# Performance work log

Hardware: AMD Instinct MI355X
Metric: run time of the kernel (lower is better)

The kernel has to match this reference:

```python
import jax, jax.numpy as jnp
import numpy as np

B, T = 2, 2048
D_MODEL, D_HIDDEN = 1024, 2048
N_EXPERTS, TOP_K = 8, 2
N_TOKENS = B * T
CAPACITY = 2 * N_TOKENS * TOP_K // N_EXPERTS  # 4096


def setup_inputs() -> dict:
    key = jax.random.key(0)
    k_x, k_rw, k_w, k_v, k_o = jax.random.split(key, 5)
    x = jax.random.normal(k_x, (B, T, D_MODEL), jnp.float32)
    # router: nn.Linear(d_model, n_experts) -> weight [E, D], bias [E]
    router_w = jax.random.normal(k_rw, (N_EXPERTS, D_MODEL), jnp.float32) * D_MODEL ** -0.5
    router_b = jnp.zeros((N_EXPERTS,), jnp.float32)
    # stacked expert params, matching SwiGLU init scales
    W = jax.random.normal(k_w, (N_EXPERTS, D_MODEL, D_HIDDEN), jnp.float32) * D_MODEL ** -0.5
    V = jax.random.normal(k_v, (N_EXPERTS, D_MODEL, D_HIDDEN), jnp.float32) * D_MODEL ** -0.5
    W_out = jax.random.normal(k_o, (N_EXPERTS, D_HIDDEN, D_MODEL), jnp.float32) * D_HIDDEN ** -0.5
    return {"x": x, "router_w": router_w, "router_b": router_b, "W": W, "V": V, "W_out": W_out}


def reference(x, router_w, router_b, W, V, W_out):
    Bq, Tq, D = x.shape
    N = Bq * Tq
    x_flat = x.reshape(N, D)

    # token-level top-k routing
    router_logits = x_flat @ router_w.T + router_b            # [N, E]
    top_vals, top_ids = jax.lax.top_k(router_logits, TOP_K)   # [N, K]
    top_probs = jax.nn.softmax(top_vals, axis=-1)             # [N, K]

    # pad row N: gathers with fill index N read zeros / contribute zero weight
    x_pad = jnp.concatenate([x_flat, jnp.zeros((1, D), x_flat.dtype)], axis=0)
    probs_pad = jnp.concatenate([top_probs, jnp.zeros((1, TOP_K), top_probs.dtype)], axis=0)

    out = jnp.zeros((N + 1, D), x_flat.dtype)
    for e in range(N_EXPERTS):  # static small loop over experts
        tok, slot = jnp.nonzero(top_ids == e, size=CAPACITY, fill_value=(N, 0))
        w = probs_pad[tok, slot][:, None]     # [C, 1], zero for padding slots
        xin = x_pad[tok]                      # [C, D] gather
        a = xin @ W[e]                        # [C, H]
        b = xin @ V[e]                        # [C, H]
        y = (a * (b * jax.nn.sigmoid(b))) @ W_out[e]  # SwiGLU: a * swish(b) -> [C, D]
        out = out.at[tok].add(y * w)          # weighted scatter-add
    return out[:N].reshape(Bq, Tq, D)
```

## Files before the change

### kernel.cpp

```cpp
#include <hip/hip_runtime.h>
#include <cstdint>
#include <cstddef>

#define N_TOK 4096
#define DM    1024
#define DH    2048
#define NE    8
#define NSLOT 8192

typedef short bf16x8_t __attribute__((ext_vector_type(8)));
typedef float f32x4    __attribute__((ext_vector_type(4)));
typedef unsigned short u16x8 __attribute__((ext_vector_type(8)));

__device__ __forceinline__ unsigned short f2bf(float f) {
  union { float f; unsigned int u; } v; v.f = f;
  unsigned int u = v.u;
  u += 0x7fffu + ((u >> 16) & 1u);
  return (unsigned short)(u >> 16);
}

#define GLD16(gp, lp)                                                          \
  __builtin_amdgcn_global_load_lds(                                            \
      (const __attribute__((address_space(1))) void*)(gp),                     \
      (__attribute__((address_space(3))) void*)(lp), 16, 0, 0)

__global__ __launch_bounds__(256) void k_transpose_bf16(
    const float* __restrict__ src0, const float* __restrict__ src1,
    unsigned short* __restrict__ dst, int R, int C,
    long srcEStride, long dstEStride, int rowOff1) {
  const int z = blockIdx.z;
  const int e = z & 7;
  const bool second = z >= 8;
  const float* s = (second ? src1 : src0) + (size_t)e * srcEStride;
  unsigned short* d = dst + (size_t)e * dstEStride + (size_t)(second ? rowOff1 : 0) * R;
  const int c0 = blockIdx.x * 64, r0 = blockIdx.y * 64;
  __shared__ float tile[64][65];
  const int t = threadIdx.x;
  {
    const int cc = (t & 15) * 4;
#pragma unroll
    for (int j = 0; j < 4; j++) {
      const int r = (t >> 4) + j * 16;
      const float4 v = *(const float4*)(s + (size_t)(r0 + r) * C + c0 + cc);
      tile[r][cc + 0] = v.x; tile[r][cc + 1] = v.y;
      tile[r][cc + 2] = v.z; tile[r][cc + 3] = v.w;
    }
  }
  __syncthreads();
  {
    const int r8 = (t & 7) * 8;
#pragma unroll
    for (int j = 0; j < 2; j++) {
      const int c = (t >> 3) + j * 32;
      u16x8 o;
#pragma unroll
      for (int i = 0; i < 8; i++) o[i] = f2bf(tile[r8 + i][c]);
      *(u16x8*)(d + (size_t)(c0 + c) * R + r0 + r8) = o;
    }
  }
}

__global__ __launch_bounds__(256) void k_router(
    const float* __restrict__ x, const float* __restrict__ rw,
    const float* __restrict__ rb, int* __restrict__ counts,
    int* __restrict__ meta_e, int* __restrict__ meta_idx,
    float* __restrict__ meta_p) {
  const int wv = threadIdx.x >> 6;
  const int l  = threadIdx.x & 63;
  const int tk = blockIdx.x * 4 + wv;
  const float* xr = x + (size_t)tk * DM;

  float acc[NE];
#pragma unroll
  for (int e = 0; e < NE; e++) acc[e] = 0.f;
#pragma unroll 4
  for (int i = 0; i < DM / 64; i++) {
    const float xv = xr[i * 64 + l];
#pragma unroll
    for (int e = 0; e < NE; e++) acc[e] += xv * rw[e * DM + i * 64 + l];
  }
#pragma unroll
  for (int off = 32; off > 0; off >>= 1) {
#pragma unroll
    for (int e = 0; e < NE; e++) acc[e] += __shfl_xor(acc[e], off);
  }
#pragma unroll
  for (int e = 0; e < NE; e++) acc[e] += rb[e];

  float v0 = -1e30f; int e0 = 0;
#pragma unroll
  for (int e = 0; e < NE; e++) { if (acc[e] > v0) { v0 = acc[e]; e0 = e; } }
  float v1 = -1e30f; int e1 = 0;
#pragma unroll
  for (int e = 0; e < NE; e++) { if (e != e0 && acc[e] > v1) { v1 = acc[e]; e1 = e; } }
  const float p0 = 1.0f / (1.0f + __expf(v1 - v0));
  const float p1 = 1.0f - p0;

  if (l == 0) {
    const int i0 = atomicAdd(&counts[e0], 1);
    const int i1 = atomicAdd(&counts[e1], 1);
    meta_e[tk * 2 + 0] = e0;  meta_e[tk * 2 + 1] = e1;
    meta_idx[tk * 2 + 0] = i0; meta_idx[tk * 2 + 1] = i1;
    meta_p[tk * 2 + 0] = p0;  meta_p[tk * 2 + 1] = p1;
  }
}

__global__ void k_prefix(const int* __restrict__ counts, int* __restrict__ offsets) {
  if (threadIdx.x == 0) {
    int s = 0;
#pragma unroll
    for (int e = 0; e < NE; e++) { offsets[e] = s; s += counts[e]; }
  }
}

__global__ __launch_bounds__(256) void k_gather(
    const float* __restrict__ x, const int* __restrict__ meta_e,
    const int* __restrict__ meta_idx, const int* __restrict__ offsets,
    unsigned short* __restrict__ Xg) {
  const int s = blockIdx.x;
  const int tk = s >> 1;
  const int e = meta_e[s];
  const int gslot = offsets[e] + meta_idx[s];
  const float4 v = ((const float4*)(x + (size_t)tk * DM))[threadIdx.x];
  ushort4 o;
  o.x = f2bf(v.x); o.y = f2bf(v.y); o.z = f2bf(v.z); o.w = f2bf(v.w);
  *(ushort4*)(Xg + (size_t)gslot * DM + threadIdx.x * 4) = o;
}

__global__ __launch_bounds__(256, 2) void k_gemm1(
    const unsigned short* __restrict__ Xg, const unsigned short* __restrict__ B1t,
    unsigned short* __restrict__ G, const int* __restrict__ counts,
    const int* __restrict__ offsets) {
  const int e = blockIdx.z;
  const int mt = blockIdx.y;
  const int cnt = counts[e];
  if (mt * 128 >= cnt) return;
  const int h0 = blockIdx.x * 128;
  const int off = offsets[e];
  const int row_base = off + mt * 128;

  __shared__ unsigned short As[128 * 32];
  __shared__ unsigned short Ws[128 * 32];
  __shared__ unsigned short Vs[128 * 32];

  const int t = threadIdx.x;
  const int l = t & 63;
  const int w = t >> 6;
  const int wm = (w >> 1) * 64;
  const int wn = (w & 1) * 64;
  const int lr = l & 15;
  const int kq = (l >> 4) * 8;

  const unsigned short* Bw = B1t + ((size_t)e * 4096 + h0) * DM;
  const unsigned short* Bv = Bw + (size_t)DH * DM;

  const int c0 = t, c1 = t + 256;
  const int ar0 = c0 >> 2, ak0 = (c0 & 3) * 8;
  const int ar1 = c1 >> 2, ak1 = (c1 & 3) * 8;
  const int arow0 = min(row_base + ar0, NSLOT - 1);
  const int arow1 = min(row_base + ar1, NSLOT - 1);

  f32x4 acc_a[4][4], acc_b[4][4];
  const f32x4 z4 = {0.f, 0.f, 0.f, 0.f};
#pragma unroll
  for (int i = 0; i < 4; i++)
#pragma unroll
    for (int j = 0; j < 4; j++) { acc_a[i][j] = z4; acc_b[i][j] = z4; }

  for (int k0 = 0; k0 < DM; k0 += 32) {
    __syncthreads();
    GLD16(Xg + (size_t)arow0 * DM + k0 + ak0, As + c0 * 8);
    GLD16(Xg + (size_t)arow1 * DM + k0 + ak1, As + c1 * 8);
    GLD16(Bw + (size_t)ar0 * DM + k0 + ak0, Ws + c0 * 8);
    GLD16(Bw + (size_t)ar1 * DM + k0 + ak1, Ws + c1 * 8);
    GLD16(Bv + (size_t)ar0 * DM + k0 + ak0, Vs + c0 * 8);
    GLD16(Bv + (size_t)ar1 * DM + k0 + ak1, Vs + c1 * 8);
    __syncthreads();

    bf16x8_t af[4], wf[4], vf[4];
#pragma unroll
    for (int mi = 0; mi < 4; mi++)
      af[mi] = *(const bf16x8_t*)&As[(wm + mi * 16 + lr) * 32 + kq];
#pragma unroll
    for (int ni = 0; ni < 4; ni++) {
      wf[ni] = *(const bf16x8_t*)&Ws[(wn + ni * 16 + lr) * 32 + kq];
      vf[ni] = *(const bf16x8_t*)&Vs[(wn + ni * 16 + lr) * 32 + kq];
    }
#pragma unroll
    for (int mi = 0; mi < 4; mi++)
#pragma unroll
      for (int ni = 0; ni < 4; ni++) {
        acc_a[mi][ni] = __builtin_amdgcn_mfma_f32_16x16x32_bf16(af[mi], wf[ni], acc_a[mi][ni], 0, 0, 0);
        acc_b[mi][ni] = __builtin_amdgcn_mfma_f32_16x16x32_bf16(af[mi], vf[ni], acc_b[mi][ni], 0, 0, 0);
      }
  }

  const int q4 = (l >> 4) * 4;
#pragma unroll
  for (int mi = 0; mi < 4; mi++) {
#pragma unroll
    for (int r = 0; r < 4; r++) {
      const int mloc = mt * 128 + wm + mi * 16 + q4 + r;
      if (mloc >= cnt) continue;
      unsigned short* grow = G + (size_t)(off + mloc) * DH;
#pragma unroll
      for (int ni = 0; ni < 4; ni++) {
        const int h = h0 + wn + ni * 16 + lr;
        const float a = acc_a[mi][ni][r];
        const float b = acc_b[mi][ni][r];
        const float s = b / (1.0f + __expf(-b));
        grow[h] = f2bf(a * s);
      }
    }
  }
}

__global__ __launch_bounds__(256, 2) void k_gemm2(
    const unsigned short* __restrict__ G, const unsigned short* __restrict__ B2t,
    float* __restrict__ Y, const int* __restrict__ counts,
    const int* __restrict__ offsets) {
  const int e = blockIdx.z;
  const int mt = blockIdx.y;
  const int cnt = counts[e];
  if (mt * 128 >= cnt) return;
  const int n0 = blockIdx.x * 128;
  const int off = offsets[e];
  const int row_base = off + mt * 128;

  __shared__ unsigned short As[128 * 32];
  __shared__ unsigned short Bs[128 * 32];

  const int t = threadIdx.x;
  const int l = t & 63;
  const int w = t >> 6;
  const int wm = (w >> 1) * 64;
  const int wn = (w & 1) * 64;
  const int lr = l & 15;
  const int kq = (l >> 4) * 8;

  const unsigned short* Bp = B2t + ((size_t)e * DM + n0) * DH;

  const int c0 = t, c1 = t + 256;
  const int ar0 = c0 >> 2, ak0 = (c0 & 3) * 8;
  const int ar1 = c1 >> 2, ak1 = (c1 & 3) * 8;
  const int arow0 = min(row_base + ar0, NSLOT - 1);
  const int arow1 = min(row_base + ar1, NSLOT - 1);

  f32x4 acc[4][4];
  const f32x4 z4 = {0.f, 0.f, 0.f, 0.f};
#pragma unroll
  for (int i = 0; i < 4; i++)
#pragma unroll
    for (int j = 0; j < 4; j++) acc[i][j] = z4;

  for (int k0 = 0; k0 < DH; k0 += 32) {
    __syncthreads();
    GLD16(G + (size_t)arow0 * DH + k0 + ak0, As + c0 * 8);
    GLD16(G + (size_t)arow1 * DH + k0 + ak1, As + c1 * 8);
    GLD16(Bp + (size_t)ar0 * DH + k0 + ak0, Bs + c0 * 8);
    GLD16(Bp + (size_t)ar1 * DH + k0 + ak1, Bs + c1 * 8);
    __syncthreads();

    bf16x8_t af[4], bf[4];
#pragma unroll
    for (int mi = 0; mi < 4; mi++)
      af[mi] = *(const bf16x8_t*)&As[(wm + mi * 16 + lr) * 32 + kq];
#pragma unroll
    for (int ni = 0; ni < 4; ni++)
      bf[ni] = *(const bf16x8_t*)&Bs[(wn + ni * 16 + lr) * 32 + kq];
#pragma unroll
    for (int mi = 0; mi < 4; mi++)
#pragma unroll
      for (int ni = 0; ni < 4; ni++)
        acc[mi][ni] = __builtin_amdgcn_mfma_f32_16x16x32_bf16(af[mi], bf[ni], acc[mi][ni], 0, 0, 0);
  }

  const int q4 = (l >> 4) * 4;
#pragma unroll
  for (int mi = 0; mi < 4; mi++) {
#pragma unroll
    for (int r = 0; r < 4; r++) {
      const int mloc = mt * 128 + wm + mi * 16 + q4 + r;
      if (mloc >= cnt) continue;
      float* yrow = Y + (size_t)(off + mloc) * DM;
#pragma unroll
      for (int ni = 0; ni < 4; ni++)
        yrow[n0 + wn + ni * 16 + lr] = acc[mi][ni][r];
    }
  }
}

__global__ __launch_bounds__(256) void k_combine(
    const float* __restrict__ Y, const int* __restrict__ meta_e,
    const int* __restrict__ meta_idx, const float* __restrict__ meta_p,
    const int* __restrict__ offsets, float* __restrict__ out) {
  const int tk = blockIdx.x;
  const int s0 = tk * 2, s1 = s0 + 1;
  const int g0 = offsets[meta_e[s0]] + meta_idx[s0];
  const int g1 = offsets[meta_e[s1]] + meta_idx[s1];
  const float w0 = meta_p[s0], w1 = meta_p[s1];
  const float4 a = ((const float4*)(Y + (size_t)g0 * DM))[threadIdx.x];
  const float4 b = ((const float4*)(Y + (size_t)g1 * DM))[threadIdx.x];
  float4 o;
  o.x = w0 * a.x + w1 * b.x;
  o.y = w0 * a.y + w1 * b.y;
  o.z = w0 * a.z + w1 * b.z;
  o.w = w0 * a.w + w1 * b.w;
  ((float4*)(out + (size_t)tk * DM))[threadIdx.x] = o;
}

extern "C" void kernel_launch(void* const* d_in, const int* in_sizes, int n_in,
                              void* d_out, int out_size, void* d_ws, size_t ws_size,
                              hipStream_t stream) {
  const float* x    = (const float*)d_in[0];
  const float* rw   = (const float*)d_in[1];
  const float* rb   = (const float*)d_in[2];
  const float* W    = (const float*)d_in[3];
  const float* V    = (const float*)d_in[4];
  const float* Wout = (const float*)d_in[5];
  float* out = (float*)d_out;

  char* p = (char*)d_ws;
  unsigned short* B1t = (unsigned short*)p; p += (size_t)NE * 4096 * DM * 2;
  float*          Y   = (float*)B1t;
  unsigned short* B2t = (unsigned short*)p; p += (size_t)NE * DM * DH * 2;
  unsigned short* Xg  = (unsigned short*)p; p += (size_t)NSLOT * DM * 2;
  unsigned short* G   = (unsigned short*)p; p += (size_t)NSLOT * DH * 2;
  int*   counts      = (int*)p;   p += 256;
  int*   offsets     = (int*)p;   p += 256;
  int*   meta_e      = (int*)p;   p += (size_t)N_TOK * 2 * 4;
  int*   meta_idx    = (int*)p;   p += (size_t)N_TOK * 2 * 4;
  float* meta_p      = (float*)p; p += (size_t)N_TOK * 2 * 4;

  hipMemsetAsync(counts, 0, 256, stream);

  k_transpose_bf16<<<dim3(DH / 64, DM / 64, 2 * NE), 256, 0, stream>>>(
      W, V, B1t, DM, DH, (long)DM * DH, (long)4096 * DM, DH);
  k_transpose_bf16<<<dim3(DM / 64, DH / 64, NE), 256, 0, stream>>>(
      Wout, Wout, B2t, DH, DM, (long)DH * DM, (long)DM * DH, 0);

  k_router<<<N_TOK / 4, 256, 0, stream>>>(x, rw, rb, counts, meta_e, meta_idx, meta_p);
  k_prefix<<<1, 64, 0, stream>>>(counts, offsets);
  k_gather<<<NSLOT, 256, 0, stream>>>(x, meta_e, meta_idx, offsets, Xg);

  k_gemm1<<<dim3(DH / 128, NSLOT / 128, NE), 256, 0, stream>>>(Xg, B1t, G, counts, offsets);
  k_gemm2<<<dim3(DM / 128, NSLOT / 128, NE), 256, 0, stream>>>(G, B2t, Y, counts, offsets);
  k_combine<<<N_TOK, 256, 0, stream>>>(Y, meta_e, meta_idx, meta_p, offsets, out);
}
```

Measured before the change: 532.9 us.

## Split-K the down-projection GEMM and fold launches into fewer kernels

Splits gemm2's K dimension into two halves written to separate Y buffers, doubling the block count for better CU occupancy, with the combine kernel summing both halves. Merges the two weight transposes into one launch that also zeroes the counts, removes the memset and the prefix kernel by computing offsets inline from counts, and gathers once per token to both slots. The split costs an extra fp32 Y buffer of write and read traffic in exchange for more parallelism and fewer launches.

```diff
diff --git a/kernel.cpp b/kernel.cpp
--- a/kernel.cpp
+++ b/kernel.cpp
@@ -24,16 +24,39 @@
       (const __attribute__((address_space(1))) void*)(gp),                     \
       (__attribute__((address_space(3))) void*)(lp), 16, 0, 0)
 
-__global__ __launch_bounds__(256) void k_transpose_bf16(
-    const float* __restrict__ src0, const float* __restrict__ src1,
-    unsigned short* __restrict__ dst, int R, int C,
-    long srcEStride, long dstEStride, int rowOff1) {
+__device__ __forceinline__ int expert_off(const int* __restrict__ counts, int e, int* cnt) {
+  int off = 0, s = 0;
+#pragma unroll
+  for (int i = 0; i < NE; i++) { if (i == e) off = s; s += counts[i]; }
+  *cnt = counts[e];
+  return off;
+}
+
+__global__ __launch_bounds__(256) void k_transpose(
+    const float* __restrict__ W, const float* __restrict__ V,
+    const float* __restrict__ Wout, unsigned short* __restrict__ B1t,
+    unsigned short* __restrict__ B2t, int* __restrict__ counts) {
+  if (blockIdx.z == 0 && blockIdx.x == 0 && blockIdx.y == 0 && threadIdx.x < NE)
+    counts[threadIdx.x] = 0;
+
   const int z = blockIdx.z;
-  const int e = z & 7;
-  const bool second = z >= 8;
-  const float* s = (second ? src1 : src0) + (size_t)e * srcEStride;
-  unsigned short* d = dst + (size_t)e * dstEStride + (size_t)(second ? rowOff1 : 0) * R;
-  const int c0 = blockIdx.x * 64, r0 = blockIdx.y * 64;
+  const float* s;
+  unsigned short* d;
+  int R, C, xt, yt;
+  if (z < 16) {
+    const int e = z & 7;
+    s = ((z < 8) ? W : V) + (size_t)e * DM * DH;
+    d = B1t + (size_t)e * 4096 * DM + (size_t)((z < 8) ? 0 : DH) * DM;
+    R = DM; C = DH; xt = blockIdx.x; yt = blockIdx.y;
+  } else {
+    const int e = z - 16;
+    s = Wout + (size_t)e * DH * DM;
+    d = B2t + (size_t)e * DM * DH;
+    R = DH; C = DM;
+    const int flat = blockIdx.x * 16 + blockIdx.y;
+    xt = flat & 15; yt = flat >> 4;
+  }
+  const int c0 = xt * 64, r0 = yt * 64;
   __shared__ float tile[64][65];
   const int t = threadIdx.x;
   {
@@ -105,38 +128,34 @@
   }
 }
 
-__global__ void k_prefix(const int* __restrict__ counts, int* __restrict__ offsets) {
-  if (threadIdx.x == 0) {
-    int s = 0;
-#pragma unroll
-    for (int e = 0; e < NE; e++) { offsets[e] = s; s += counts[e]; }
-  }
-}
-
 __global__ __launch_bounds__(256) void k_gather(
     const float* __restrict__ x, const int* __restrict__ meta_e,
-    const int* __restrict__ meta_idx, const int* __restrict__ offsets,
+    const int* __restrict__ meta_idx, const int* __restrict__ counts,
     unsigned short* __restrict__ Xg) {
-  const int s = blockIdx.x;
-  const int tk = s >> 1;
-  const int e = meta_e[s];
-  const int gslot = offsets[e] + meta_idx[s];
+  const int tk = blockIdx.x;
+  int offs[NE];
+  { int s = 0;
+#pragma unroll
+    for (int e = 0; e < NE; e++) { offs[e] = s; s += counts[e]; } }
+  const int s0 = tk * 2, s1 = s0 + 1;
+  const int g0 = offs[meta_e[s0]] + meta_idx[s0];
+  const int g1 = offs[meta_e[s1]] + meta_idx[s1];
   const float4 v = ((const float4*)(x + (size_t)tk * DM))[threadIdx.x];
   ushort4 o;
   o.x = f2bf(v.x); o.y = f2bf(v.y); o.z = f2bf(v.z); o.w = f2bf(v.w);
-  *(ushort4*)(Xg + (size_t)gslot * DM + threadIdx.x * 4) = o;
+  *(ushort4*)(Xg + (size_t)g0 * DM + threadIdx.x * 4) = o;
+  *(ushort4*)(Xg + (size_t)g1 * DM + threadIdx.x * 4) = o;
 }
 
 __global__ __launch_bounds__(256, 2) void k_gemm1(
     const unsigned short* __restrict__ Xg, const unsigned short* __restrict__ B1t,
-    unsigned short* __restrict__ G, const int* __restrict__ counts,
-    const int* __restrict__ offsets) {
+    unsigned short* __restrict__ G, const int* __restrict__ counts) {
   const int e = blockIdx.z;
+  int cnt;
+  const int off = expert_off(counts, e, &cnt);
   const int mt = blockIdx.y;
-  const int cnt = counts[e];
   if (mt * 128 >= cnt) return;
   const int h0 = blockIdx.x * 128;
-  const int off = offsets[e];
   const int row_base = off + mt * 128;
 
   __shared__ unsigned short As[128 * 32];
@@ -217,15 +236,17 @@
 
 __global__ __launch_bounds__(256, 2) void k_gemm2(
     const unsigned short* __restrict__ G, const unsigned short* __restrict__ B2t,
-    float* __restrict__ Y, const int* __restrict__ counts,
-    const int* __restrict__ offsets) {
-  const int e = blockIdx.z;
+    float* __restrict__ Y, const int* __restrict__ counts) {
+  const int z = blockIdx.z;
+  const int e = z & 7;
+  const int half = z >> 3;
+  int cnt;
+  const int off = expert_off(counts, e, &cnt);
   const int mt = blockIdx.y;
-  const int cnt = counts[e];
   if (mt * 128 >= cnt) return;
   const int n0 = blockIdx.x * 128;
-  const int off = offsets[e];
   const int row_base = off + mt * 128;
+  const int kbase = half * 1024;
 
   __shared__ unsigned short As[128 * 32];
   __shared__ unsigned short Bs[128 * 32];
@@ -253,7 +274,8 @@
 #pragma unroll
     for (int j = 0; j < 4; j++) acc[i][j] = z4;
 
-  for (int k0 = 0; k0 < DH; k0 += 32) {
+  for (int kk = 0; kk < 1024; kk += 32) {
+    const int k0 = kbase + kk;
     __syncthreads();
     GLD16(G + (size_t)arow0 * DH + k0 + ak0, As + c0 * 8);
     GLD16(G + (size_t)arow1 * DH + k0 + ak1, As + c1 * 8);
@@ -275,6 +297,7 @@
         acc[mi][ni] = __builtin_amdgcn_mfma_f32_16x16x32_bf16(af[mi], bf[ni], acc[mi][ni], 0, 0, 0);
   }
 
+  float* Yh = Y + (size_t)half * NSLOT * DM;
   const int q4 = (l >> 4) * 4;
 #pragma unroll
   for (int mi = 0; mi < 4; mi++) {
@@ -282,7 +305,7 @@
     for (int r = 0; r < 4; r++) {
       const int mloc = mt * 128 + wm + mi * 16 + q4 + r;
       if (mloc >= cnt) continue;
-      float* yrow = Y + (size_t)(off + mloc) * DM;
+      float* yrow = Yh + (size_t)(off + mloc) * DM;
 #pragma unroll
       for (int ni = 0; ni < 4; ni++)
         yrow[n0 + wn + ni * 16 + lr] = acc[mi][ni][r];
@@ -293,19 +316,26 @@
 __global__ __launch_bounds__(256) void k_combine(
     const float* __restrict__ Y, const int* __restrict__ meta_e,
     const int* __restrict__ meta_idx, const float* __restrict__ meta_p,
-    const int* __restrict__ offsets, float* __restrict__ out) {
+    const int* __restrict__ counts, float* __restrict__ out) {
   const int tk = blockIdx.x;
+  int offs[NE];
+  { int s = 0;
+#pragma unroll
+    for (int e = 0; e < NE; e++) { offs[e] = s; s += counts[e]; } }
   const int s0 = tk * 2, s1 = s0 + 1;
-  const int g0 = offsets[meta_e[s0]] + meta_idx[s0];
-  const int g1 = offsets[meta_e[s1]] + meta_idx[s1];
+  const int g0 = offs[meta_e[s0]] + meta_idx[s0];
+  const int g1 = offs[meta_e[s1]] + meta_idx[s1];
   const float w0 = meta_p[s0], w1 = meta_p[s1];
-  const float4 a = ((const float4*)(Y + (size_t)g0 * DM))[threadIdx.x];
-  const float4 b = ((const float4*)(Y + (size_t)g1 * DM))[threadIdx.x];
+  const float* Y1 = Y + (size_t)NSLOT * DM;
+  const float4 a0 = ((const float4*)(Y  + (size_t)g0 * DM))[threadIdx.x];
+  const float4 a1 = ((const float4*)(Y1 + (size_t)g0 * DM))[threadIdx.x];
+  const float4 b0 = ((const float4*)(Y  + (size_t)g1 * DM))[threadIdx.x];
+  const float4 b1 = ((const float4*)(Y1 + (size_t)g1 * DM))[threadIdx.x];
   float4 o;
-  o.x = w0 * a.x + w1 * b.x;
-  o.y = w0 * a.y + w1 * b.y;
-  o.z = w0 * a.z + w1 * b.z;
-  o.w = w0 * a.w + w1 * b.w;
+  o.x = w0 * (a0.x + a1.x) + w1 * (b0.x + b1.x);
+  o.y = w0 * (a0.y + a1.y) + w1 * (b0.y + b1.y);
+  o.z = w0 * (a0.z + a1.z) + w1 * (b0.z + b1.z);
+  o.w = w0 * (a0.w + a1.w) + w1 * (b0.w + b1.w);
   ((float4*)(out + (size_t)tk * DM))[threadIdx.x] = o;
 }
 
@@ -327,23 +357,14 @@
   unsigned short* Xg  = (unsigned short*)p; p += (size_t)NSLOT * DM * 2;
   unsigned short* G   = (unsigned short*)p; p += (size_t)NSLOT * DH * 2;
   int*   counts      = (int*)p;   p += 256;
-  int*   offsets     = (int*)p;   p += 256;
   int*   meta_e      = (int*)p;   p += (size_t)N_TOK * 2 * 4;
   int*   meta_idx    = (int*)p;   p += (size_t)N_TOK * 2 * 4;
   float* meta_p      = (float*)p; p += (size_t)N_TOK * 2 * 4;
 
-  hipMemsetAsync(counts, 0, 256, stream);
-
-  k_transpose_bf16<<<dim3(DH / 64, DM / 64, 2 * NE), 256, 0, stream>>>(
-      W, V, B1t, DM, DH, (long)DM * DH, (long)4096 * DM, DH);
-  k_transpose_bf16<<<dim3(DM / 64, DH / 64, NE), 256, 0, stream>>>(
-      Wout, Wout, B2t, DH, DM, (long)DH * DM, (long)DM * DH, 0);
-
+  k_transpose<<<dim3(32, 16, 24), 256, 0, stream>>>(W, V, Wout, B1t, B2t, counts);
   k_router<<<N_TOK / 4, 256, 0, stream>>>(x, rw, rb, counts, meta_e, meta_idx, meta_p);
-  k_prefix<<<1, 64, 0, stream>>>(counts, offsets);
-  k_gather<<<NSLOT, 256, 0, stream>>>(x, meta_e, meta_idx, offsets, Xg);
-
-  k_gemm1<<<dim3(DH / 128, NSLOT / 128, NE), 256, 0, stream>>>(Xg, B1t, G, counts, offsets);
-  k_gemm2<<<dim3(DM / 128, NSLOT / 128, NE), 256, 0, stream>>>(G, B2t, Y, counts, offsets);
-  k_combine<<<N_TOK, 256, 0, stream>>>(Y, meta_e, meta_idx, meta_p, offsets, out);
-}
+  k_gather<<<N_TOK, 256, 0, stream>>>(x, meta_e, meta_idx, counts, Xg);
+  k_gemm1<<<dim3(DH / 128, NSLOT / 128, NE), 256, 0, stream>>>(Xg, B1t, G, counts);
+  k_gemm2<<<dim3(DM / 128, NSLOT / 128, 2 * NE), 256, 0, stream>>>(G, B2t, Y, counts);
+  k_combine<<<N_TOK, 256, 0, stream>>>(Y, meta_e, meta_idx, meta_p, counts, out);
+}
```

Result: faster. 516.2 us (-3.1%).
